# Optimization experiments

Hardware: AMD Instinct MI355X
Metric: run time of the kernel (lower is better)

Reference implementation:

```python
import math
import jax, jax.numpy as jnp
import numpy as np

N_HEAD = 16

def rms_norm(x, w, eps=1e-6):
    x32 = x.astype(jnp.float32)
    ms = jnp.mean(x32 * x32, axis=-1, keepdims=True)
    y = (x32 * jax.lax.rsqrt(ms + eps)).astype(x.dtype)
    return y * w

def apply_rope(x, cos, sin):
    # x: [B,H,S,D], cos/sin: [S,D/2] broadcast over B,H
    half = x.shape[-1] // 2
    x1, x2 = x[..., :half], x[..., half:]
    return jnp.concatenate((x1 * cos - x2 * sin, x2 * cos + x1 * sin), axis=-1).astype(x.dtype)

def setup_inputs() -> dict:
    key = jax.random.key(0)
    ks = jax.random.split(key, 8)
    B, S, D = 1, 4096, 1024
    hd = D // N_HEAD
    x = jax.random.normal(ks[0], (B, S, D), dtype=jnp.float32)
    # rotary embeddings
    inv_freq = 1.0 / (10000.0 ** (jnp.arange(0, hd, 2, dtype=jnp.float32) / hd))  # [hd/2]
    ang = jnp.arange(S, dtype=jnp.float32)[:, None] * inv_freq  # [S, hd/2]
    cos, sin = jnp.cos(ang), jnp.sin(ang)
    # additive causal mask [1,1,S,S]
    causal = jnp.tril(jnp.ones((S, S), dtype=bool))
    attention_mask = jnp.where(causal, 0.0, -1e9).astype(jnp.float32)[None, None]
    init = 0.02
    wq = jax.random.normal(ks[1], (D, D), dtype=jnp.float32) * init
    wk = jax.random.normal(ks[2], (D, D), dtype=jnp.float32) * init
    wv = jax.random.normal(ks[3], (D, D), dtype=jnp.float32) * init
    wo = jax.random.normal(ks[4], (D, D), dtype=jnp.float32) * init
    q_norm_w = jnp.ones((hd,), dtype=jnp.float32)
    k_norm_w = jnp.ones((hd,), dtype=jnp.float32)
    return {"x": x, "cos": cos, "sin": sin, "attention_mask": attention_mask,
            "wq": wq, "wk": wk, "wv": wv, "wo": wo,
            "q_norm_w": q_norm_w, "k_norm_w": k_norm_w}

def reference(x, cos, sin, attention_mask, wq, wk, wv, wo, q_norm_w, k_norm_w):
    B, S, D = x.shape
    H = N_HEAD
    hd = D // H
    q = (x @ wq.T).reshape(B, S, H, hd)
    k = (x @ wk.T).reshape(B, S, H, hd)
    v = (x @ wv.T).reshape(B, S, H, hd)
    q = jnp.swapaxes(rms_norm(q, q_norm_w), 1, 2)  # [B,H,S,hd]
    k = jnp.swapaxes(rms_norm(k, k_norm_w), 1, 2)
    v = jnp.swapaxes(v, 1, 2)
    q = apply_rope(q, cos, sin)
    k = apply_rope(k, cos, sin)
    scores = jnp.einsum('bhqd,bhkd->bhqk', q, k) / math.sqrt(hd)
    scores = scores + attention_mask
    attn = jax.nn.softmax(scores.astype(jnp.float32), axis=-1).astype(q.dtype)
    o = jnp.einsum('bhqk,bhkd->bhqd', attn, v)  # [B,H,S,hd]
    o = jnp.swapaxes(o, 1, 2).reshape(B, S, D)
    return o @ wo.T
```

## Files before the change

### kernel.cpp

```cpp
#include <hip/hip_runtime.h>

#define S_LEN 4096
#define DIM   1024
#define NH    16
#define HD    64

typedef __bf16 bf16;
typedef __attribute__((ext_vector_type(8)))  __bf16 bf16x8;
typedef __attribute__((ext_vector_type(4)))  float  f32x4;
typedef __attribute__((ext_vector_type(16))) float  f32x16;
typedef __attribute__((ext_vector_type(4)))  unsigned int uint4v;

typedef __attribute__((address_space(3))) void lds_void;
typedef __attribute__((address_space(1))) void g_void;

#if __has_builtin(__builtin_amdgcn_exp2f)
#define EXP2(x) __builtin_amdgcn_exp2f(x)
#else
#define EXP2(x) exp2f(x)
#endif

__device__ __forceinline__ void gl_lds16(const void* g, void* l) {
    __builtin_amdgcn_global_load_lds((g_void*)(void*)g, (lds_void*)l, 16, 0, 0);
}

__device__ __forceinline__ unsigned int pk2(float a, float b) {
    unsigned short ua = __builtin_bit_cast(unsigned short, (bf16)a);
    unsigned short ub = __builtin_bit_cast(unsigned short, (bf16)b);
    return (unsigned int)ua | ((unsigned int)ub << 16);
}

__device__ __forceinline__ int ksw23(int x) {
    return (x & ~12) | ((x & 8) >> 1) | ((x & 4) << 1);
}

__global__ __launch_bounds__(256) void f2b_all(
    const float* __restrict__ x,  const float* __restrict__ wq,
    const float* __restrict__ wk, const float* __restrict__ wv,
    const float* __restrict__ wo,
    bf16* __restrict__ xb, bf16* __restrict__ wqkv, bf16* __restrict__ wob)
{
    int b = blockIdx.x;
    const float* src; bf16* dst; int base;
    if (b < 2048)      { src = x;  dst = xb;              base = b; }
    else if (b < 2560) { src = wq; dst = wqkv;            base = b - 2048; }
    else if (b < 3072) { src = wk; dst = wqkv + 1048576;  base = b - 2560; }
    else if (b < 3584) { src = wv; dst = wqkv + 2097152;  base = b - 3072; }
    else               { src = wo; dst = wob;             base = b - 3584; }
    int i = base * 2048 + threadIdx.x * 8;
    float4 a = *(const float4*)(src + i);
    float4 c = *(const float4*)(src + i + 4);
    bf16x8 r;
    r[0]=(bf16)a.x; r[1]=(bf16)a.y; r[2]=(bf16)a.z; r[3]=(bf16)a.w;
    r[4]=(bf16)c.x; r[5]=(bf16)c.y; r[6]=(bf16)c.z; r[7]=(bf16)c.w;
    *(bf16x8*)(dst + i) = r;
}

__global__ __launch_bounds__(256) void gemm_qkv(
    const bf16* __restrict__ A, const bf16* __restrict__ B,
    bf16* __restrict__ outQ, bf16* __restrict__ outK, bf16* __restrict__ outV,
    const float* __restrict__ cosb, const float* __restrict__ sinb,
    const float* __restrict__ qw,   const float* __restrict__ kw)
{
    const int K = 1024;
    __shared__ bf16 As[128][32];
    __shared__ bf16 Bs[128][32];
    const int bm = blockIdx.x, bn = blockIdx.y;
    const int tid  = threadIdx.x;
    const int wave = tid >> 6, lane = tid & 63;
    const int g = lane >> 4, r = lane & 15;
    const int wr = wave >> 1, wc = wave & 1;
    const int rr = lane >> 2, cc = (lane & 3) * 8;

    f32x4 acc[4][4] = {};

    const bf16* Ab = A + (size_t)(bm * 128) * K;
    const bf16* Bb = B + (size_t)(bn * 128) * K;

    for (int k0 = 0; k0 < K; k0 += 32) {
        #pragma unroll
        for (int i = 0; i < 2; ++i) {
            gl_lds16(Ab + (size_t)(wave*32 + i*16 + rr) * K + k0 + cc, &As[wave*32 + i*16][0]);
            gl_lds16(Bb + (size_t)(wave*32 + i*16 + rr) * K + k0 + cc, &Bs[wave*32 + i*16][0]);
        }
        __syncthreads();
        bf16x8 a[4], b[4];
        #pragma unroll
        for (int m = 0; m < 4; ++m) a[m] = *(const bf16x8*)&As[wr*64 + m*16 + r][g*8];
        #pragma unroll
        for (int n = 0; n < 4; ++n) b[n] = *(const bf16x8*)&Bs[wc*64 + n*16 + r][g*8];
        #pragma unroll
        for (int m = 0; m < 4; ++m)
            #pragma unroll
            for (int n = 0; n < 4; ++n)
                acc[m][n] = __builtin_amdgcn_mfma_f32_16x16x32_bf16(a[m], b[n], acc[m][n], 0, 0, 0);
        __syncthreads();
    }

    if (bn >= 16) {
        #pragma unroll
        for (int m = 0; m < 4; ++m)
            #pragma unroll
            for (int n = 0; n < 4; ++n)
                #pragma unroll
                for (int i = 0; i < 4; ++i) {
                    int row = bm*128 + wr*64 + m*16 + g*4 + i;
                    int col = bn*128 + wc*64 + n*16 + r;
                    int c2 = col - 2048;
                    int hh = c2 >> 6, d = c2 & 63;
                    int pos = ksw23(row & 63) ^ ((d & 7) << 3);
                    outV[((size_t)(hh * HD + d)) * S_LEN + (row & ~63) + pos] = (bf16)acc[m][n][i];
                }
    } else {
        const bool isK = (bn >= 8);
        const float* wn = isK ? kw : qw;
        bf16* dst = isK ? outK : outQ;
        const int h = ((bn & 7) << 1) | wc;
        float wv4[4];
        #pragma unroll
        for (int n = 0; n < 4; ++n) wv4[n] = wn[n * 16 + r];
        #pragma unroll
        for (int m = 0; m < 4; ++m)
            #pragma unroll
            for (int i = 0; i < 4; ++i) {
                int srow = bm*128 + wr*64 + m*16 + g*4 + i;
                float ss = acc[m][0][i]*acc[m][0][i] + acc[m][1][i]*acc[m][1][i]
                         + acc[m][2][i]*acc[m][2][i] + acc[m][3][i]*acc[m][3][i];
                ss += __shfl_xor(ss, 1);
                ss += __shfl_xor(ss, 2);
                ss += __shfl_xor(ss, 4);
                ss += __shfl_xor(ss, 8);
                float rn = rsqrtf(ss * (1.0f / 64.0f) + 1e-6f);
                float xn0 = acc[m][0][i] * rn * wv4[0];
                float xn1 = acc[m][1][i] * rn * wv4[1];
                float xn2 = acc[m][2][i] * rn * wv4[2];
                float xn3 = acc[m][3][i] * rn * wv4[3];
                float c0 = cosb[srow * 32 + r],      c1 = cosb[srow * 32 + 16 + r];
                float s0 = sinb[srow * 32 + r],      s1 = sinb[srow * 32 + 16 + r];
                float y0 = xn0 * c0 - xn2 * s0;
                float y1 = xn1 * c1 - xn3 * s1;
                float y2 = xn2 * c0 + xn0 * s0;
                float y3 = xn3 * c1 + xn1 * s1;
                size_t ob = ((size_t)h * S_LEN + srow) * HD;
                if (isK) {
                    int sw = (srow & 7) << 3;
                    dst[ob + ((     r) ^ sw)] = (bf16)y0;
                    dst[ob + ((16 + r) ^ sw)] = (bf16)y1;
                    dst[ob + ((32 + r) ^ sw)] = (bf16)y2;
                    dst[ob + ((48 + r) ^ sw)] = (bf16)y3;
                } else {
                    dst[ob +      r] = (bf16)y0;
                    dst[ob + 16 + r] = (bf16)y1;
                    dst[ob + 32 + r] = (bf16)y2;
                    dst[ob + 48 + r] = (bf16)y3;
                }
            }
    }
}

__global__ __launch_bounds__(256) void gemm_out(
    const bf16* __restrict__ A, const bf16* __restrict__ B,
    float* __restrict__ outF)
{
    const int K = 1024, N = 1024;
    __shared__ bf16 As[64][32];
    __shared__ bf16 Bs[128][32];
    const int bm = blockIdx.x, bn = blockIdx.y;
    const int tid  = threadIdx.x;
    const int wave = tid >> 6, lane = tid & 63;
    const int g = lane >> 4, r = lane & 15;
    const int wr = wave >> 1, wc = wave & 1;
    const int rr = lane >> 2, cc = (lane & 3) * 8;

    f32x4 acc[2][4] = {};

    const bf16* Ab = A + (size_t)(bm * 64) * K;
    const bf16* Bb = B + (size_t)(bn * 128) * K;

    for (int k0 = 0; k0 < K; k0 += 32) {
        gl_lds16(Ab + (size_t)(wave*16 + rr) * K + k0 + cc, &As[wave*16][0]);
        #pragma unroll
        for (int i = 0; i < 2; ++i)
            gl_lds16(Bb + (size_t)(wave*32 + i*16 + rr) * K + k0 + cc, &Bs[wave*32 + i*16][0]);
        __syncthreads();
        bf16x8 a[2], b[4];
        #pragma unroll
        for (int m = 0; m < 2; ++m) a[m] = *(const bf16x8*)&As[wr*32 + m*16 + r][g*8];
        #pragma unroll
        for (int n = 0; n < 4; ++n) b[n] = *(const bf16x8*)&Bs[wc*64 + n*16 + r][g*8];
        #pragma unroll
        for (int m = 0; m < 2; ++m)
            #pragma unroll
            for (int n = 0; n < 4; ++n)
                acc[m][n] = __builtin_amdgcn_mfma_f32_16x16x32_bf16(a[m], b[n], acc[m][n], 0, 0, 0);
        __syncthreads();
    }

    #pragma unroll
    for (int m = 0; m < 2; ++m)
        #pragma unroll
        for (int n = 0; n < 4; ++n)
            #pragma unroll
            for (int i = 0; i < 4; ++i) {
                int row = bm*64 + wr*32 + m*16 + g*4 + i;
                int col = bn*128 + wc*64 + n*16 + r;
                outF[(size_t)row * N + col] = acc[m][n][i];
            }
}

__global__ __launch_bounds__(256, 4) void attn_kernel(
    const bf16* __restrict__ q, const bf16* __restrict__ k,
    const bf16* __restrict__ vt,
    bf16* __restrict__ Opc, float* __restrict__ lpc)
{
    __shared__ bf16 Ks[2][64][64];
    __shared__ bf16 Vt[2][64][64];

    const int idx = blockIdx.x;
    const int h = idx & 15;
    const int u = idx >> 4;
    const int qt = 31 - (u >> 2);
    const int c  = u & 3;
    const int nt = 2 * qt + 2;
    const int t0 = (c * nt) >> 2;
    const int t1 = ((c + 1) * nt) >> 2;

    const int q0 = qt * 128;
    const int tid = threadIdx.x;
    const int wave = tid >> 6, lane = tid & 63;
    const int l31 = lane & 31, hi = lane >> 5;

    const bf16* qh  = q  + (size_t)h * S_LEN * HD;
    const bf16* kh  = k  + (size_t)h * S_LEN * HD;
    const bf16* vth = vt + (size_t)h * HD * S_LEN;

    const int qrow = q0 + wave * 32 + l31;
    bf16x8 qf[4];
    #pragma unroll
    for (int ds4 = 0; ds4 < 4; ++ds4)
        qf[ds4] = *(const bf16x8*)(qh + (size_t)qrow * HD + ds4 * 16 + hi * 8);

    float l_run = 0.f;
    f32x16 acc_o[2] = {};

    const int srow = lane >> 3, scol = (lane & 7) * 8;
    const float C1 = 0.125f * 1.44269504088896f;
    const float C2 = 8.0f * 1.44269504088896f;

    auto stage = [&](int t, int buf) {
        const int k0 = t * 64;
        const bf16* kb = kh + (size_t)(k0 + wave * 16) * HD;
        gl_lds16(kb + (size_t)(srow    ) * HD + scol, &Ks[buf][wave * 16][0]);
        gl_lds16(kb + (size_t)(srow + 8) * HD + scol, &Ks[buf][wave * 16 + 8][0]);
        const bf16* vb = vth + (size_t)(wave * 16) * S_LEN + k0;
        gl_lds16(vb + (size_t)(srow    ) * S_LEN + scol, &Vt[buf][wave * 16][0]);
        gl_lds16(vb + (size_t)(srow + 8) * S_LEN + scol, &Vt[buf][wave * 16 + 8][0]);
    };

#define COMPUTE_TILE(T, BUF)                                                  \
    do {                                                                      \
        const int k0_ = (T) * 64;                                             \
        const bool masked_ = ((T) >= 2 * qt);                                 \
        f32x16 sacc_[2];                                                      \
        __builtin_amdgcn_s_setprio(1);                                        \
        _Pragma("unroll")                                                     \
        for (int kn = 0; kn < 2; ++kn) {                                      \
            const int krow = kn * 32 + l31;                                   \
            const int sw = (krow & 7) << 3;                                   \
            f32x16 z = {};                                                    \
            _Pragma("unroll")                                                 \
            for (int ds4 = 0; ds4 < 4; ++ds4) {                               \
                bf16x8 kfr = *(const bf16x8*)&Ks[BUF][krow][(ds4 * 16 + hi * 8) ^ sw]; \
                z = __builtin_amdgcn_mfma_f32_32x32x16_bf16(kfr, qf[ds4], z, 0, 0, 0); \
            }                                                                 \
            sacc_[kn] = z;                                                    \
        }                                                                     \
        __builtin_amdgcn_s_setprio(0);                                        \
        float p_[32];                                                         \
        _Pragma("unroll")                                                     \
        for (int kn = 0; kn < 2; ++kn)                                        \
            _Pragma("unroll")                                                 \
            for (int rg = 0; rg < 16; ++rg) {                                 \
                float e = EXP2(fmaf(sacc_[kn][rg], C1, -C2));                 \
                if (masked_) {                                                \
                    int kloc = kn * 32 + (rg & 3) + 8 * (rg >> 2) + 4 * hi;   \
                    if (k0_ + kloc > qrow) e = 0.f;                           \
                }                                                             \
                p_[kn * 16 + rg] = e;                                         \
            }                                                                 \
        float s0_ = 0.f, s1_ = 0.f, s2_ = 0.f, s3_ = 0.f;                     \
        _Pragma("unroll")                                                     \
        for (int j = 0; j < 8; ++j) {                                         \
            s0_ += p_[4*j];   s1_ += p_[4*j+1];                               \
            s2_ += p_[4*j+2]; s3_ += p_[4*j+3];                               \
        }                                                                     \
        float rs_ = (s0_ + s1_) + (s2_ + s3_);                                \
        rs_ += __shfl_xor(rs_, 32);                                           \
        l_run += rs_;                                                         \
        bf16x8 pa_[4];                                                        \
        _Pragma("unroll")                                                     \
        for (int ks4 = 0; ks4 < 4; ++ks4) {                                   \
            uint4v w_;                                                        \
            w_.x = pk2(p_[8*ks4+0], p_[8*ks4+1]);                             \
            w_.y = pk2(p_[8*ks4+2], p_[8*ks4+3]);                             \
            w_.z = pk2(p_[8*ks4+4], p_[8*ks4+5]);                             \
            w_.w = pk2(p_[8*ks4+6], p_[8*ks4+7]);                             \
            pa_[ks4] = __builtin_bit_cast(bf16x8, w_);                        \
        }                                                                     \
        __builtin_amdgcn_s_setprio(1);                                        \
        _Pragma("unroll")                                                     \
        for (int n = 0; n < 2; ++n) {                                         \
            const int d = n * 32 + l31;                                       \
            const int sw = (d & 7) << 3;                                      \
            f32x16 a = acc_o[n];                                              \
            _Pragma("unroll")                                                 \
            for (int ks4 = 0; ks4 < 4; ++ks4) {                               \
                bf16x8 vfr = *(const bf16x8*)&Vt[BUF][d][(ks4 * 16 + hi * 8) ^ sw]; \
                a = __builtin_amdgcn_mfma_f32_32x32x16_bf16(pa_[ks4], vfr, a, 0, 0, 0); \
            }                                                                 \
            acc_o[n] = a;                                                     \
        }                                                                     \
        __builtin_amdgcn_s_setprio(0);                                        \
    } while (0)

    if (t0 < t1) {
        stage(t0, 0);
        asm volatile("s_waitcnt vmcnt(0)" ::: "memory");
        __syncthreads();
        int t = t0;
        while (t + 2 <= t1) {
            stage(t + 1, 1);
            COMPUTE_TILE(t, 0);
            asm volatile("s_waitcnt vmcnt(0)" ::: "memory");
            __syncthreads();
            if (t + 2 < t1) stage(t + 2, 0);
            COMPUTE_TILE(t + 1, 1);
            asm volatile("s_waitcnt vmcnt(0)" ::: "memory");
            __syncthreads();
            t += 2;
        }
        if (t < t1) COMPUTE_TILE(t, 0);
    }
#undef COMPUTE_TILE

    bf16* Op = Opc + (size_t)c * S_LEN * DIM;
    #pragma unroll
    for (int n = 0; n < 2; ++n)
        #pragma unroll
        for (int rg = 0; rg < 16; ++rg) {
            int s_abs = q0 + wave * 32 + (rg & 3) + 8 * (rg >> 2) + 4 * hi;
            Op[(size_t)s_abs * DIM + h * HD + n * 32 + l31] = (bf16)acc_o[n][rg];
        }
    if (lane < 32)
        lpc[c * (NH * S_LEN) + h * S_LEN + (q0 + wave * 32 + lane)] = l_run;
}

__global__ __launch_bounds__(256) void combine_kernel(
    const bf16* __restrict__ Opc, const float* __restrict__ lpc,
    bf16* __restrict__ o)
{
    int gid = blockIdx.x * 256 + threadIdx.x;
    int e = gid * 8;
    int s = e >> 10, h = (e & 1023) >> 6;
    float a[8] = {};
    #pragma unroll
    for (int c = 0; c < 4; ++c) {
        bf16x8 v = *(const bf16x8*)(Opc + (size_t)c * S_LEN * DIM + e);
        #pragma unroll
        for (int j = 0; j < 8; ++j) a[j] += (float)v[j];
    }
    float l = 0.f;
    #pragma unroll
    for (int c = 0; c < 4; ++c) l += lpc[c * (NH * S_LEN) + h * S_LEN + s];
    float inv = __builtin_amdgcn_rcpf(l);
    bf16x8 rv;
    #pragma unroll
    for (int j = 0; j < 8; ++j) rv[j] = (bf16)(a[j] * inv);
    *(bf16x8*)(o + e) = rv;
}

extern "C" void kernel_launch(void* const* d_in, const int* in_sizes, int n_in,
                              void* d_out, int out_size, void* d_ws, size_t ws_size,
                              hipStream_t stream)
{
    const float* x    = (const float*)d_in[0];
    const float* cosb = (const float*)d_in[1];
    const float* sinb = (const float*)d_in[2];
    const float* wq   = (const float*)d_in[4];
    const float* wk   = (const float*)d_in[5];
    const float* wv   = (const float*)d_in[6];
    const float* wo   = (const float*)d_in[7];
    const float* qw   = (const float*)d_in[8];
    const float* kw   = (const float*)d_in[9];

    char* ws = (char*)d_ws;
    const size_t MB = 1024 * 1024;
    bf16*  wob   = (bf16*)(ws + 0);
    bf16*  q_ws  = (bf16*)(ws + 2 * MB);
    bf16*  k_ws  = (bf16*)(ws + 10 * MB);
    bf16*  vt_ws = (bf16*)(ws + 18 * MB);
    bf16*  Opc   = (bf16*)(ws + 26 * MB);
    bf16*  o_ws  = (bf16*)(ws + 26 * MB);
    bf16*  xb    = (bf16*)(ws + 26 * MB);
    bf16*  wqkv  = (bf16*)(ws + 34 * MB);
    float* lpc   = (float*)(ws + 58 * MB);

    f2b_all<<<4096, 256, 0, stream>>>(x, wq, wk, wv, wo, xb, wqkv, wob);

    gemm_qkv<<<dim3(32, 24), 256, 0, stream>>>(xb, wqkv, q_ws, k_ws, vt_ws,
                                               cosb, sinb, qw, kw);
    attn_kernel<<<2048, 256, 0, stream>>>(q_ws, k_ws, vt_ws, Opc, lpc);
    combine_kernel<<<4096 * 1024 / 8 / 256, 256, 0, stream>>>(Opc, lpc, o_ws);
    gemm_out<<<dim3(64, 8), 256, 0, stream>>>(o_ws, wob, (float*)d_out);
}
```

Baseline: 145.6 us.

## Fuse split-K attention combine into output projection GEMM A-tile load

Removes the separate combine kernel and instead has the output GEMM sum the four partial attention outputs and normalize them by the summed row denominators while loading each A tile into shared memory. The GEMM M-tile is doubled to 128 rows, giving 256 blocks instead of 512, so each block reuses the B tile across more rows. This avoids one kernel launch and an 8MB intermediate write and read. In exchange, the A loads become synchronous register-path loads that read four times the bytes per tile, the grid is smaller, and register pressure is higher.

Measured after the change: 162.8 us. +11.8%, slower.

```diff
diff --git a/kernel.cpp b/kernel.cpp
--- a/kernel.cpp
+++ b/kernel.cpp
@@ -158,12 +158,12 @@
     }
 }
 
-__global__ __launch_bounds__(256) void gemm_out(
-    const bf16* __restrict__ A, const bf16* __restrict__ B,
-    float* __restrict__ outF)
+__global__ __launch_bounds__(256) void gemm_out_fused(
+    const bf16* __restrict__ Opc, const float* __restrict__ lpc,
+    const bf16* __restrict__ B, float* __restrict__ outF)
 {
     const int K = 1024, N = 1024;
-    __shared__ bf16 As[64][32];
+    __shared__ bf16 As[128][32];
     __shared__ bf16 Bs[128][32];
     const int bm = blockIdx.x, bn = blockIdx.y;
     const int tid  = threadIdx.x;
@@ -172,24 +172,54 @@
     const int wr = wave >> 1, wc = wave & 1;
     const int rr = lane >> 2, cc = (lane & 3) * 8;
 
-    f32x4 acc[2][4] = {};
-
-    const bf16* Ab = A + (size_t)(bm * 64) * K;
+    f32x4 acc[4][4] = {};
+
+    const int s0 = bm * 128 + wave * 32 + rr;
+    const int s1 = s0 + 16;
     const bf16* Bb = B + (size_t)(bn * 128) * K;
 
+    float inv0 = 0.f, inv1 = 0.f;
+
     for (int k0 = 0; k0 < K; k0 += 32) {
-        gl_lds16(Ab + (size_t)(wave*16 + rr) * K + k0 + cc, &As[wave*16][0]);
+        if ((k0 & 63) == 0) {
+            int h = k0 >> 6;
+            float l0 = 0.f, l1 = 0.f;
+            #pragma unroll
+            for (int c = 0; c < 4; ++c) {
+                l0 += lpc[c * (NH * S_LEN) + h * S_LEN + s0];
+                l1 += lpc[c * (NH * S_LEN) + h * S_LEN + s1];
+            }
+            inv0 = __builtin_amdgcn_rcpf(l0);
+            inv1 = __builtin_amdgcn_rcpf(l1);
+        }
+        #pragma unroll
+        for (int i = 0; i < 2; ++i) {
+            const int s = i ? s1 : s0;
+            const float inv = i ? inv1 : inv0;
+            float sum[8] = {};
+            #pragma unroll
+            for (int c = 0; c < 4; ++c) {
+                bf16x8 v = *(const bf16x8*)(Opc + (size_t)c * S_LEN * DIM
+                                            + (size_t)s * DIM + k0 + cc);
+                #pragma unroll
+                for (int j = 0; j < 8; ++j) sum[j] += (float)v[j];
+            }
+            bf16x8 y;
+            #pragma unroll
+            for (int j = 0; j < 8; ++j) y[j] = (bf16)(sum[j] * inv);
+            *(bf16x8*)&As[wave * 32 + i * 16 + rr][cc] = y;
+        }
         #pragma unroll
         for (int i = 0; i < 2; ++i)
             gl_lds16(Bb + (size_t)(wave*32 + i*16 + rr) * K + k0 + cc, &Bs[wave*32 + i*16][0]);
         __syncthreads();
-        bf16x8 a[2], b[4];
-        #pragma unroll
-        for (int m = 0; m < 2; ++m) a[m] = *(const bf16x8*)&As[wr*32 + m*16 + r][g*8];
+        bf16x8 a[4], b[4];
+        #pragma unroll
+        for (int m = 0; m < 4; ++m) a[m] = *(const bf16x8*)&As[wr*64 + m*16 + r][g*8];
         #pragma unroll
         for (int n = 0; n < 4; ++n) b[n] = *(const bf16x8*)&Bs[wc*64 + n*16 + r][g*8];
         #pragma unroll
-        for (int m = 0; m < 2; ++m)
+        for (int m = 0; m < 4; ++m)
             #pragma unroll
             for (int n = 0; n < 4; ++n)
                 acc[m][n] = __builtin_amdgcn_mfma_f32_16x16x32_bf16(a[m], b[n], acc[m][n], 0, 0, 0);
@@ -197,12 +227,12 @@
     }
 
     #pragma unroll
-    for (int m = 0; m < 2; ++m)
+    for (int m = 0; m < 4; ++m)
         #pragma unroll
         for (int n = 0; n < 4; ++n)
             #pragma unroll
             for (int i = 0; i < 4; ++i) {
-                int row = bm*64 + wr*32 + m*16 + g*4 + i;
+                int row = bm*128 + wr*64 + m*16 + g*4 + i;
                 int col = bn*128 + wc*64 + n*16 + r;
                 outF[(size_t)row * N + col] = acc[m][n][i];
             }
@@ -355,30 +385,6 @@
         lpc[c * (NH * S_LEN) + h * S_LEN + (q0 + wave * 32 + lane)] = l_run;
 }
 
-__global__ __launch_bounds__(256) void combine_kernel(
-    const bf16* __restrict__ Opc, const float* __restrict__ lpc,
-    bf16* __restrict__ o)
-{
-    int gid = blockIdx.x * 256 + threadIdx.x;
-    int e = gid * 8;
-    int s = e >> 10, h = (e & 1023) >> 6;
-    float a[8] = {};
-    #pragma unroll
-    for (int c = 0; c < 4; ++c) {
-        bf16x8 v = *(const bf16x8*)(Opc + (size_t)c * S_LEN * DIM + e);
-        #pragma unroll
-        for (int j = 0; j < 8; ++j) a[j] += (float)v[j];
-    }
-    float l = 0.f;
-    #pragma unroll
-    for (int c = 0; c < 4; ++c) l += lpc[c * (NH * S_LEN) + h * S_LEN + s];
-    float inv = __builtin_amdgcn_rcpf(l);
-    bf16x8 rv;
-    #pragma unroll
-    for (int j = 0; j < 8; ++j) rv[j] = (bf16)(a[j] * inv);
-    *(bf16x8*)(o + e) = rv;
-}
-
 extern "C" void kernel_launch(void* const* d_in, const int* in_sizes, int n_in,
                               void* d_out, int out_size, void* d_ws, size_t ws_size,
                               hipStream_t stream)
@@ -400,7 +406,6 @@
     bf16*  k_ws  = (bf16*)(ws + 10 * MB);
     bf16*  vt_ws = (bf16*)(ws + 18 * MB);
     bf16*  Opc   = (bf16*)(ws + 26 * MB);
-    bf16*  o_ws  = (bf16*)(ws + 26 * MB);
     bf16*  xb    = (bf16*)(ws + 26 * MB);
     bf16*  wqkv  = (bf16*)(ws + 34 * MB);
     float* lpc   = (float*)(ws + 58 * MB);
@@ -410,6 +415,5 @@
     gemm_qkv<<<dim3(32, 24), 256, 0, stream>>>(xb, wqkv, q_ws, k_ws, vt_ws,
                                                cosb, sinb, qw, kw);
     attn_kernel<<<2048, 256, 0, stream>>>(q_ws, k_ws, vt_ws, Opc, lpc);
-    combine_kernel<<<4096 * 1024 / 8 / 256, 256, 0, stream>>>(Opc, lpc, o_ws);
-    gemm_out<<<dim3(64, 8), 256, 0, stream>>>(o_ws, wob, (float*)d_out);
-}
+    gemm_out_fused<<<dim3(32, 8), 256, 0, stream>>>(Opc, lpc, wob, (float*)d_out);
+}
```
